# Optimization experiments

Hardware: AMD Instinct MI355X
Metric: run time of the kernel (lower is better)

The kernel has to match this reference:

```python
import jax, jax.numpy as jnp
import numpy as np

B, S, D, H = 1, 4096, 1024, 16
HD = D // H  # head_dim = 64


def setup_inputs() -> dict:
    key = jax.random.key(0)
    k1, k2, k3 = jax.random.split(key, 3)
    scale = 0.02
    return {
        "x": jax.random.normal(k1, (B, S, D), dtype=jnp.float32),
        "w_qkv": jax.random.normal(k2, (D, 3 * D), dtype=jnp.float32) * scale,
        "b_qkv": jnp.zeros((3 * D,), dtype=jnp.float32),
        "w_proj": jax.random.normal(k3, (D, D), dtype=jnp.float32) * scale,
        "b_proj": jnp.zeros((D,), dtype=jnp.float32),
    }


def reference(x, w_qkv, b_qkv, w_proj, b_proj):
    b, s, d = x.shape
    qkv = x @ w_qkv + b_qkv                      # [b, s, 3d]
    q, k, v = jnp.split(qkv, 3, axis=-1)
    # [b, h, s, hd]
    q = q.reshape(b, s, H, HD).transpose(0, 2, 1, 3)
    k = k.reshape(b, s, H, HD).transpose(0, 2, 1, 3)
    v = v.reshape(b, s, H, HD).transpose(0, 2, 1, 3)
    score = jnp.einsum("bhqd,bhkd->bhqk", q, k) / jnp.sqrt(jnp.float32(HD))
    causal = jnp.tril(jnp.ones((s, s), dtype=bool))
    score = jnp.where(causal, score, -jnp.inf)
    attn = jax.nn.softmax(score, axis=-1)        # dropout omitted (eval mode, p effectively 0)
    out = jnp.einsum("bhqk,bhkd->bhqd", attn, v)  # [b, h, s, hd]
    out = out.transpose(0, 2, 1, 3).reshape(b, s, d)
    return out @ w_proj + b_proj
```

## Files before the change

### kernel.cpp

```cpp
#include <hip/hip_runtime.h>
#include <hip/hip_bf16.h>
#include <math.h>

typedef __bf16 bf16;
typedef __bf16 bf16x8 __attribute__((ext_vector_type(8)));
typedef __bf16 bf16x4 __attribute__((ext_vector_type(4)));
typedef float f32x4 __attribute__((ext_vector_type(4)));

#define S_ 4096
#define D_ 1024
#define H_ 16
#define HD_ 64
#define N3_ 3072
#define NSPLIT 2

typedef const __attribute__((address_space(1))) void* gas1_t;
typedef __attribute__((address_space(3))) void* las3_t;
static __device__ __forceinline__ void g2l16(const void* g, void* l) {
  __builtin_amdgcn_global_load_lds((gas1_t)g, (las3_t)l, 16, 0, 0);
}

__global__ __launch_bounds__(256) void prep_kernel(const float* __restrict__ x,
                                                   bf16* __restrict__ xb,
                                                   const float* __restrict__ w_qkv,
                                                   bf16* __restrict__ wqkvT,
                                                   const float* __restrict__ w_proj,
                                                   bf16* __restrict__ wprojT) {
  __shared__ float t[32][33];
  const int b = blockIdx.x;
  if (b < 4096) {
    int i = (b * 256 + threadIdx.x) * 4;
    float4 v = *(const float4*)(x + i);
    bf16x4 o;
    o.x = (bf16)v.x; o.y = (bf16)v.y; o.z = (bf16)v.z; o.w = (bf16)v.w;
    *(bf16x4*)(xb + i) = o;
    return;
  }
  const float* in; bf16* outp; int ldin, bx, by;
  if (b < 7168) { int b2 = b - 4096; in = w_qkv;  outp = wqkvT;  ldin = N3_; bx = (b2 % 96) * 32; by = (b2 / 96) * 32; }
  else          { int b3 = b - 7168; in = w_proj; outp = wprojT; ldin = D_;  bx = (b3 % 32) * 32; by = (b3 / 32) * 32; }
  const int tx = threadIdx.x & 31, ty = threadIdx.x >> 5;
#pragma unroll
  for (int i = 0; i < 4; ++i)
    t[ty + i * 8][tx] = in[(size_t)(by + ty + i * 8) * ldin + bx + tx];
  __syncthreads();
#pragma unroll
  for (int i = 0; i < 4; ++i)
    outp[(size_t)(bx + ty + i * 8) * D_ + by + tx] = (bf16)t[tx][ty + i * 8];
}

__global__ __launch_bounds__(512, 2) void gemm256_qkv(const bf16* __restrict__ A,
                                                      const bf16* __restrict__ Bt,
                                                      const float* __restrict__ bias,
                                                      bf16* __restrict__ outb,
                                                      bf16* __restrict__ vTout,
                                                      float qscale) {
  __shared__ bf16 smem[65536];
  const int K = D_;
  const int NTK = K / 64;
  const int tid = threadIdx.x;
  const int lane = tid & 63, wv = tid >> 6;
  const int col = lane & 15, quad = lane >> 4;
  const int wr = wv >> 2, wc = wv & 3;
  const long bm = (long)blockIdx.x * 256, bn = (long)blockIdx.y * 256;

  int srowA[2][2], srowB[2][2];
  int schA[2][2], schB[2][2];
#pragma unroll
  for (int q = 0; q < 2; ++q) {
    int slot = q * 512 + tid;
    int rl = slot >> 3, ch = slot & 7;
#pragma unroll
    for (int h = 0; h < 2; ++h) {
      int rowA = (rl & 63) | (h << 6) | ((rl >> 6) << 7);
      srowA[h][q] = rowA; schA[h][q] = ch ^ (rowA & 7);
      int rowB = (rl & 31) | (h << 5) | ((rl >> 5) << 6);
      srowB[h][q] = rowB; schB[h][q] = ch ^ (rowB & 7);
    }
  }
  const int dstoff = tid * 8;

  const int ck[2] = { ((0 * 4 + quad) ^ (col & 7)) * 8, ((1 * 4 + quad) ^ (col & 7)) * 8 };

#define STAGE_A(h, T, buf)                                                        \
  {                                                                               \
    const int kbs = (T) * 64;                                                     \
    bf16* lb = smem + (buf) * 32768 + (h) * 8192;                                 \
    g2l16(A + (bm + srowA[h][0]) * (long)K + kbs + schA[h][0] * 8, lb + dstoff);  \
    g2l16(A + (bm + srowA[h][1]) * (long)K + kbs + schA[h][1] * 8, lb + 4096 + dstoff); \
  }
#define STAGE_B(h, T, buf)                                                        \
  {                                                                               \
    const int kbs = (T) * 64;                                                     \
    bf16* lb = smem + (buf) * 32768 + 16384 + (h) * 8192;                         \
    g2l16(Bt + (bn + srowB[h][0]) * (long)K + kbs + schB[h][0] * 8, lb + dstoff); \
    g2l16(Bt + (bn + srowB[h][1]) * (long)K + kbs + schB[h][1] * 8, lb + 4096 + dstoff); \
  }

  f32x4 acc[8][4] = {};

  STAGE_A(0, 0, 0);
  STAGE_A(1, 0, 0);
  STAGE_B(0, 0, 0);
  STAGE_A(0, 1, 1);
  STAGE_B(1, 0, 0);

  for (int G = 0; G < NTK; ++G) {
    const int cur = G & 1;
    const bf16* bufc = smem + cur * 32768;
    const bool last = (G == NTK - 1);

    bf16x8 afr[4][2], bfr[2][2][2];

    if (last) asm volatile("s_waitcnt vmcnt(2)" ::: "memory");
    else      asm volatile("s_waitcnt vmcnt(4)" ::: "memory");
    __builtin_amdgcn_s_barrier();
    __builtin_amdgcn_sched_barrier(0);
#pragma unroll
    for (int mt = 0; mt < 4; ++mt) {
      const bf16* rp = bufc + (wr * 64 + mt * 16 + col) * 64;
      afr[mt][0] = *(const bf16x8*)(rp + ck[0]);
      afr[mt][1] = *(const bf16x8*)(rp + ck[1]);
    }
#pragma unroll
    for (int nt = 0; nt < 2; ++nt) {
      const bf16* rp = bufc + 16384 + (wc * 32 + nt * 16 + col) * 64;
      bfr[0][nt][0] = *(const bf16x8*)(rp + ck[0]);
      bfr[0][nt][1] = *(const bf16x8*)(rp + ck[1]);
    }
    if (G + 1 < NTK) STAGE_A(1, G + 1, cur ^ 1);
    asm volatile("s_waitcnt lgkmcnt(0)" ::: "memory");
    __builtin_amdgcn_sched_barrier(0);
    __builtin_amdgcn_s_setprio(1);
#pragma unroll
    for (int mt = 0; mt < 4; ++mt)
#pragma unroll
      for (int nt = 0; nt < 2; ++nt) {
        acc[mt][nt] = __builtin_amdgcn_mfma_f32_16x16x32_bf16(afr[mt][0], bfr[0][nt][0], acc[mt][nt], 0, 0, 0);
        acc[mt][nt] = __builtin_amdgcn_mfma_f32_16x16x32_bf16(afr[mt][1], bfr[0][nt][1], acc[mt][nt], 0, 0, 0);
      }
    __builtin_amdgcn_s_setprio(0);

    if (last) asm volatile("s_waitcnt vmcnt(0)" ::: "memory");
    else      asm volatile("s_waitcnt vmcnt(2)" ::: "memory");
    __builtin_amdgcn_s_barrier();
    __builtin_amdgcn_sched_barrier(0);
#pragma unroll
    for (int nt = 0; nt < 2; ++nt) {
      const bf16* rp = bufc + 16384 + 8192 + (wc * 32 + nt * 16 + col) * 64;
      bfr[1][nt][0] = *(const bf16x8*)(rp + ck[0]);
      bfr[1][nt][1] = *(const bf16x8*)(rp + ck[1]);
    }
    if (G + 1 < NTK) STAGE_B(0, G + 1, cur ^ 1);
    asm volatile("s_waitcnt lgkmcnt(0)" ::: "memory");
    __builtin_amdgcn_sched_barrier(0);
    __builtin_amdgcn_s_setprio(1);
#pragma unroll
    for (int mt = 0; mt < 4; ++mt)
#pragma unroll
      for (int nt = 0; nt < 2; ++nt) {
        acc[mt][2 + nt] = __builtin_amdgcn_mfma_f32_16x16x32_bf16(afr[mt][0], bfr[1][nt][0], acc[mt][2 + nt], 0, 0, 0);
        acc[mt][2 + nt] = __builtin_amdgcn_mfma_f32_16x16x32_bf16(afr[mt][1], bfr[1][nt][1], acc[mt][2 + nt], 0, 0, 0);
      }
    __builtin_amdgcn_s_setprio(0);

    __builtin_amdgcn_s_barrier();
    __builtin_amdgcn_sched_barrier(0);
#pragma unroll
    for (int mt = 0; mt < 4; ++mt) {
      const bf16* rp = bufc + 8192 + (wr * 64 + mt * 16 + col) * 64;
      afr[mt][0] = *(const bf16x8*)(rp + ck[0]);
      afr[mt][1] = *(const bf16x8*)(rp + ck[1]);
    }
    if (G + 2 < NTK) STAGE_A(0, G + 2, cur);
    asm volatile("s_waitcnt lgkmcnt(0)" ::: "memory");
    __builtin_amdgcn_sched_barrier(0);
    __builtin_amdgcn_s_setprio(1);
#pragma unroll
    for (int mt = 0; mt < 4; ++mt)
#pragma unroll
      for (int nt = 0; nt < 2; ++nt) {
        acc[4 + mt][2 + nt] = __builtin_amdgcn_mfma_f32_16x16x32_bf16(afr[mt][0], bfr[1][nt][0], acc[4 + mt][2 + nt], 0, 0, 0);
        acc[4 + mt][2 + nt] = __builtin_amdgcn_mfma_f32_16x16x32_bf16(afr[mt][1], bfr[1][nt][1], acc[4 + mt][2 + nt], 0, 0, 0);
      }
    __builtin_amdgcn_s_setprio(0);

    __builtin_amdgcn_s_barrier();
    __builtin_amdgcn_sched_barrier(0);
    if (G + 1 < NTK) STAGE_B(1, G + 1, cur ^ 1);
    __builtin_amdgcn_s_setprio(1);
#pragma unroll
    for (int mt = 0; mt < 4; ++mt)
#pragma unroll
      for (int nt = 0; nt < 2; ++nt) {
        acc[4 + mt][nt] = __builtin_amdgcn_mfma_f32_16x16x32_bf16(afr[mt][0], bfr[0][nt][0], acc[4 + mt][nt], 0, 0, 0);
        acc[4 + mt][nt] = __builtin_amdgcn_mfma_f32_16x16x32_bf16(afr[mt][1], bfr[0][nt][1], acc[4 + mt][nt], 0, 0, 0);
      }
    __builtin_amdgcn_s_setprio(0);
  }

  const bool isV = (blockIdx.y >= 8);
  const bool isQ = (blockIdx.y < 4);
#pragma unroll
  for (int mh = 0; mh < 2; ++mh)
#pragma unroll
    for (int mt = 0; mt < 4; ++mt)
#pragma unroll
      for (int nh = 0; nh < 2; ++nh)
#pragma unroll
        for (int nt = 0; nt < 2; ++nt) {
          long gn = bn + wc * 64 + nh * 32 + nt * 16 + col;
          float bv = bias[gn];
          long gm0 = bm + wr * 128 + mh * 64 + mt * 16 + quad * 4;
          f32x4 a = acc[mh * 4 + mt][nh * 2 + nt];
          if (isV) {
            bf16x4 vv;
#pragma unroll
            for (int i = 0; i < 4; ++i) vv[i] = (bf16)(a[i] + bv);
            *(bf16x4*)(&vTout[(gn - 2 * D_) * (long)S_ + gm0]) = vv;
          } else {
            float sc = isQ ? qscale : 1.0f;
#pragma unroll
            for (int i = 0; i < 4; ++i)
              outb[(gm0 + i) * (long)N3_ + gn] = (bf16)((a[i] + bv) * sc);
          }
        }
#undef STAGE_A
#undef STAGE_B
}

__device__ __forceinline__ int swz_g(int row) {
  return (row & 3) | ((((row >> 2) ^ (row >> 3)) & 1) << 2);
}

__global__ __launch_bounds__(256) void attn_kernel(const bf16* __restrict__ qkv,
                                                   const bf16* __restrict__ vT,
                                                   bf16* __restrict__ Opart,
                                                   float* __restrict__ lws) {
  __shared__ bf16 sK[4][64 * 64];
  __shared__ bf16 sV[4][64 * 64];
  const int bid = blockIdx.x;
  const int wgid = (bid & 7) * 128 + (bid >> 3);
  const int hh = wgid >> 6;
  const int rem = wgid & 63;
  const int qb = 31 - (rem >> 1);
  const int sp = rem & 1;
  const int tid = threadIdx.x;
  const int wave = tid >> 6, lane = tid & 63;
  const int col = lane & 15, quad = lane >> 4;
  const int qbase = qb * 128 + wave * 32;

  const bf16* qp0 = qkv + (size_t)(qbase + col) * N3_ + hh * HD_;
  bf16x8 aq[2][2];
  aq[0][0] = *(const bf16x8*)(qp0 + quad * 8);
  aq[0][1] = *(const bf16x8*)(qp0 + 32 + quad * 8);
  aq[1][0] = *(const bf16x8*)(qp0 + 16 * N3_ + quad * 8);
  aq[1][1] = *(const bf16x8*)(qp0 + 16 * N3_ + 32 + quad * 8);

  bf16x8 ones;
#pragma unroll
  for (int j = 0; j < 8; ++j) ones[j] = (bf16)1.0f;

  f32x4 acc[2][4] = {};
  f32x4 acc_l[2] = {};

  const bf16* kgbase = qkv + D_ + hh * HD_;
  const bf16* vgbase = vT + (size_t)hh * HD_ * S_;
  const int krow = (col >> 2) * 8 + (col & 3);
  const int niter = 2 * (qb + 1);
  const int len = niter / NSPLIT;
  const int it0 = sp * len;
  const int it1 = it0 + len;

  const int srow = tid >> 2;
  const int sc0 = (tid & 3) * 2;
  const int gs = swz_g(srow);
  const int soff0 = srow * 64 + ((sc0 ^ gs) * 8);
  const int soff1 = srow * 64 + (((sc0 + 1) ^ gs) * 8);

  {
    const bf16* kg = kgbase + (size_t)(it0 * 64 + srow) * N3_ + sc0 * 8;
    const bf16* vg = vgbase + (size_t)srow * S_ + it0 * 64 + sc0 * 8;
    *(int4*)(&sK[0][soff0]) = *(const int4*)kg;
    *(int4*)(&sK[0][soff1]) = *(const int4*)(kg + 8);
    *(int4*)(&sV[0][soff0]) = *(const int4*)vg;
    *(int4*)(&sV[0][soff1]) = *(const int4*)(vg + 8);
    if (it0 + 1 < it1) {
      const bf16* kg1 = kg + (size_t)64 * N3_;
      const bf16* vg1 = vg + 64;
      *(int4*)(&sK[1][soff0]) = *(const int4*)kg1;
      *(int4*)(&sK[1][soff1]) = *(const int4*)(kg1 + 8);
      *(int4*)(&sV[1][soff0]) = *(const int4*)vg1;
      *(int4*)(&sV[1][soff1]) = *(const int4*)(vg1 + 8);
    }
  }
  __syncthreads();

#define CHUNK_BODY(KB, BI)                                                        \
  if ((KB) < qbase + 32) {                                                        \
    const bool act0 = (KB) < qbase + 16;                                          \
    const bf16* kc = &sK[BI][0];                                                  \
    const bf16* vc = &sV[BI][0];                                                  \
    f32x4 st[2][4];                                                               \
    _Pragma("unroll")                                                             \
    for (int t = 0; t < 4; ++t) {                                                 \
      int row = (t >> 1) * 32 + (t & 1) * 4 + krow;                               \
      int pc = quad ^ swz_g(row);                                                 \
      bf16x8 kf0 = *(const bf16x8*)(kc + row * 64 + pc * 8);                      \
      bf16x8 kf1 = *(const bf16x8*)(kc + row * 64 + (pc ^ 4) * 8);                \
      if (act0) {                                                                 \
        f32x4 z = {};                                                             \
        z = __builtin_amdgcn_mfma_f32_16x16x32_bf16(kf0, aq[0][0], z, 0, 0, 0);   \
        st[0][t] = __builtin_amdgcn_mfma_f32_16x16x32_bf16(kf1, aq[0][1], z, 0, 0, 0); \
      }                                                                           \
      f32x4 z = {};                                                               \
      z = __builtin_amdgcn_mfma_f32_16x16x32_bf16(kf0, aq[1][0], z, 0, 0, 0);     \
      st[1][t] = __builtin_amdgcn_mfma_f32_16x16x32_bf16(kf1, aq[1][1], z, 0, 0, 0); \
    }                                                                             \
    bf16x8 pfrag[2][2];                                                           \
    _Pragma("unroll")                                                             \
    for (int s2 = 0; s2 < 2; ++s2) {                                              \
      if (s2 == 0 && !act0) continue;                                             \
      const int rowbase = qbase + 16 * s2;                                        \
      float p[4][4];                                                              \
      if ((KB) + 63 <= rowbase) {                                                 \
        _Pragma("unroll")                                                         \
        for (int t = 0; t < 4; ++t)                                               \
          _Pragma("unroll")                                                       \
          for (int r = 0; r < 4; ++r)                                             \
            p[t][r] = __builtin_amdgcn_exp2f(st[s2][t][r]);                       \
      } else {                                                                    \
        _Pragma("unroll")                                                         \
        for (int t = 0; t < 4; ++t)                                               \
          _Pragma("unroll")                                                       \
          for (int r = 0; r < 4; ++r) {                                           \
            int key = (KB) + (t >> 1) * 32 + quad * 8 + (t & 1) * 4 + r;          \
            p[t][r] = (key > rowbase + col) ? 0.f                                 \
                                            : __builtin_amdgcn_exp2f(st[s2][t][r]); \
          }                                                                       \
      }                                                                           \
      _Pragma("unroll")                                                           \
      for (int c = 0; c < 2; ++c)                                                 \
        _Pragma("unroll")                                                         \
        for (int j2 = 0; j2 < 4; ++j2) {                                          \
          pfrag[s2][c][j2]     = (bf16)p[2 * c][j2];                              \
          pfrag[s2][c][j2 + 4] = (bf16)p[2 * c + 1][j2];                          \
        }                                                                         \
    }                                                                             \
    _Pragma("unroll")                                                             \
    for (int c = 0; c < 2; ++c) {                                                 \
      _Pragma("unroll")                                                           \
      for (int n = 0; n < 4; ++n) {                                               \
        int row = n * 16 + col;                                                   \
        int pc = (4 * c + quad) ^ swz_g(row);                                     \
        bf16x8 vf = *(const bf16x8*)(vc + row * 64 + pc * 8);                     \
        if (act0)                                                                 \
          acc[0][n] = __builtin_amdgcn_mfma_f32_16x16x32_bf16(pfrag[0][c], vf, acc[0][n], 0, 0, 0); \
        acc[1][n] = __builtin_amdgcn_mfma_f32_16x16x32_bf16(pfrag[1][c], vf, acc[1][n], 0, 0, 0);   \
      }                                                                           \
      if (act0)                                                                   \
        acc_l[0] = __builtin_amdgcn_mfma_f32_16x16x32_bf16(pfrag[0][c], ones, acc_l[0], 0, 0, 0);   \
      acc_l[1] = __builtin_amdgcn_mfma_f32_16x16x32_bf16(pfrag[1][c], ones, acc_l[1], 0, 0, 0);     \
    }                                                                             \
  }

  for (int j0 = it0; j0 < it1; j0 += 2) {
    const int bb = (((j0 - it0) >> 1) & 1) * 2;
    const bool hasB = (j0 + 1 < it1);
    const bool pfA = (j0 + 2 < it1);
    const bool pfB = (j0 + 3 < it1);

    int4 nk00, nk01, nv00, nv01, nk10, nk11, nv10, nv11;
    if (pfA) {
      const bf16* kg = kgbase + (size_t)((j0 + 2) * 64 + srow) * N3_ + sc0 * 8;
      const bf16* vg = vgbase + (size_t)srow * S_ + (j0 + 2) * 64 + sc0 * 8;
      nk00 = *(const int4*)kg; nk01 = *(const int4*)(kg + 8);
      nv00 = *(const int4*)vg; nv01 = *(const int4*)(vg + 8);
    }
    if (pfB) {
      const bf16* kg = kgbase + (size_t)((j0 + 3) * 64 + srow) * N3_ + sc0 * 8;
      const bf16* vg = vgbase + (size_t)srow * S_ + (j0 + 3) * 64 + sc0 * 8;
      nk10 = *(const int4*)kg; nk11 = *(const int4*)(kg + 8);
      nv10 = *(const int4*)vg; nv11 = *(const int4*)(vg + 8);
    }

    {
      const int kb0 = j0 * 64;
      CHUNK_BODY(kb0, bb);
    }
    if (hasB) {
      const int kb1 = (j0 + 1) * 64;
      CHUNK_BODY(kb1, bb + 1);
    }

    if (pfA) {
      bf16* kn = &sK[bb ^ 2][0];
      bf16* vn = &sV[bb ^ 2][0];
      *(int4*)(kn + soff0) = nk00; *(int4*)(kn + soff1) = nk01;
      *(int4*)(vn + soff0) = nv00; *(int4*)(vn + soff1) = nv01;
    }
    if (pfB) {
      bf16* kn = &sK[(bb ^ 2) + 1][0];
      bf16* vn = &sV[(bb ^ 2) + 1][0];
      *(int4*)(kn + soff0) = nk10; *(int4*)(kn + soff1) = nk11;
      *(int4*)(vn + soff0) = nv10; *(int4*)(vn + soff1) = nv11;
    }
    __syncthreads();
  }
#undef CHUNK_BODY

  bf16* Op = Opart + (size_t)sp * S_ * D_;
#pragma unroll
  for (int s2 = 0; s2 < 2; ++s2) {
    const int rowbase = qbase + 16 * s2;
    if (col == 0) {
#pragma unroll
      for (int r = 0; r < 4; ++r)
        lws[((size_t)sp * H_ + hh) * S_ + rowbase + quad * 4 + r] = acc_l[s2][r];
    }
#pragma unroll
    for (int n = 0; n < 4; ++n)
#pragma unroll
      for (int r = 0; r < 4; ++r)
        Op[(size_t)(rowbase + quad * 4 + r) * D_ + hh * HD_ + n * 16 + col] =
            (bf16)acc[s2][n][r];
  }
}

__global__ __launch_bounds__(256) void attn_combine(const bf16* __restrict__ Opart,
                                                    const float* __restrict__ lws,
                                                    bf16* __restrict__ outb) {
  int e = (blockIdx.x * 256 + threadIdx.x) * 8;
  int s = e >> 10;
  int h = (e & (D_ - 1)) >> 6;
  float l = 0.f;
#pragma unroll
  for (int sp = 0; sp < NSPLIT; ++sp) l += lws[((size_t)sp * H_ + h) * S_ + s];
  float inv = 1.0f / l;
  float o[8] = {};
#pragma unroll
  for (int sp = 0; sp < NSPLIT; ++sp) {
    bf16x8 a = *(const bf16x8*)(Opart + (size_t)sp * S_ * D_ + e);
#pragma unroll
    for (int j = 0; j < 8; ++j) o[j] += (float)a[j];
  }
  bf16x8 r;
#pragma unroll
  for (int j = 0; j < 8; ++j) r[j] = (bf16)(o[j] * inv);
  *(bf16x8*)(outb + e) = r;
}

__global__ __launch_bounds__(256, 2) void proj8_gemm(const bf16* __restrict__ A,
                                                     const bf16* __restrict__ Bt,
                                                     const float* __restrict__ bias,
                                                     float* __restrict__ outf) {
  __shared__ bf16 smem[32768];
  const int K = D_;
  const int NTK = K / 64;
  const int tid = threadIdx.x;
  const int lane = tid & 63, wv = tid >> 6;
  const int col = lane & 15, quad = lane >> 4;
  const int wr = wv >> 1, wc = wv & 1;
  const long bm = (long)blockIdx.x * 128, bn = (long)blockIdx.y * 128;

  int srow[2][2], sch[2][2];
#pragma unroll
  for (int q = 0; q < 2; ++q) {
    int slot = q * 256 + tid;
    int rl = slot >> 3, ch = slot & 7;
#pragma unroll
    for (int h = 0; h < 2; ++h) {
      int row = (rl & 31) | (h << 5) | ((rl >> 5) << 6);
      srow[h][q] = row; sch[h][q] = ch ^ (row & 7);
    }
  }
  const int dstoff = tid * 8;

  const int ck[2] = { ((0 * 4 + quad) ^ (col & 7)) * 8, ((1 * 4 + quad) ^ (col & 7)) * 8 };

#define STAGE_PA(h, T, buf)                                                      \
  {                                                                              \
    const int kbs = (T) * 64;                                                    \
    bf16* lb = smem + (buf) * 16384 + (h) * 4096;                                \
    g2l16(A + (bm + srow[h][0]) * (long)K + kbs + sch[h][0] * 8, lb + dstoff);   \
    g2l16(A + (bm + srow[h][1]) * (long)K + kbs + sch[h][1] * 8, lb + 2048 + dstoff); \
  }
#define STAGE_PB(h, T, buf)                                                      \
  {                                                                              \
    const int kbs = (T) * 64;                                                    \
    bf16* lb = smem + (buf) * 16384 + 8192 + (h) * 4096;                         \
    g2l16(Bt + (bn + srow[h][0]) * (long)K + kbs + sch[h][0] * 8, lb + dstoff);  \
    g2l16(Bt + (bn + srow[h][1]) * (long)K + kbs + sch[h][1] * 8, lb + 2048 + dstoff); \
  }

  f32x4 acc[4][4] = {};

  STAGE_PA(0, 0, 0);
  STAGE_PA(1, 0, 0);
  STAGE_PB(0, 0, 0);
  STAGE_PA(0, 1, 1);
  STAGE_PB(1, 0, 0);

  for (int G = 0; G < NTK; ++G) {
    const int cur = G & 1;
    const bf16* bufc = smem + cur * 16384;
    const bool last = (G == NTK - 1);

    bf16x8 afr[2][2], bfr[2][2][2];

    if (last) asm volatile("s_waitcnt vmcnt(2)" ::: "memory");
    else      asm volatile("s_waitcnt vmcnt(4)" ::: "memory");
    __builtin_amdgcn_s_barrier();
    __builtin_amdgcn_sched_barrier(0);
#pragma unroll
    for (int mt = 0; mt < 2; ++mt) {
      const bf16* rp = bufc + (wr * 32 + mt * 16 + col) * 64;
      afr[mt][0] = *(const bf16x8*)(rp + ck[0]);
      afr[mt][1] = *(const bf16x8*)(rp + ck[1]);
    }
#pragma unroll
    for (int nt = 0; nt < 2; ++nt) {
      const bf16* rp = bufc + 8192 + (wc * 32 + nt * 16 + col) * 64;
      bfr[0][nt][0] = *(const bf16x8*)(rp + ck[0]);
      bfr[0][nt][1] = *(const bf16x8*)(rp + ck[1]);
    }
    if (G + 1 < NTK) STAGE_PA(1, G + 1, cur ^ 1);
    asm volatile("s_waitcnt lgkmcnt(0)" ::: "memory");
    __builtin_amdgcn_sched_barrier(0);
    __builtin_amdgcn_s_setprio(1);
#pragma unroll
    for (int mt = 0; mt < 2; ++mt)
#pragma unroll
      for (int nt = 0; nt < 2; ++nt) {
        acc[mt][nt] = __builtin_amdgcn_mfma_f32_16x16x32_bf16(afr[mt][0], bfr[0][nt][0], acc[mt][nt], 0, 0, 0);
        acc[mt][nt] = __builtin_amdgcn_mfma_f32_16x16x32_bf16(afr[mt][1], bfr[0][nt][1], acc[mt][nt], 0, 0, 0);
      }
    __builtin_amdgcn_s_setprio(0);

    if (last) asm volatile("s_waitcnt vmcnt(0)" ::: "memory");
    else      asm volatile("s_waitcnt vmcnt(2)" ::: "memory");
    __builtin_amdgcn_s_barrier();
    __builtin_amdgcn_sched_barrier(0);
#pragma unroll
    for (int nt = 0; nt < 2; ++nt) {
      const bf16* rp = bufc + 8192 + 4096 + (wc * 32 + nt * 16 + col) * 64;
      bfr[1][nt][0] = *(const bf16x8*)(rp + ck[0]);
      bfr[1][nt][1] = *(const bf16x8*)(rp + ck[1]);
    }
    if (G + 1 < NTK) STAGE_PB(0, G + 1, cur ^ 1);
    asm volatile("s_waitcnt lgkmcnt(0)" ::: "memory");
    __builtin_amdgcn_sched_barrier(0);
    __builtin_amdgcn_s_setprio(1);
#pragma unroll
    for (int mt = 0; mt < 2; ++mt)
#pragma unroll
      for (int nt = 0; nt < 2; ++nt) {
        acc[mt][2 + nt] = __builtin_amdgcn_mfma_f32_16x16x32_bf16(afr[mt][0], bfr[1][nt][0], acc[mt][2 + nt], 0, 0, 0);
        acc[mt][2 + nt] = __builtin_amdgcn_mfma_f32_16x16x32_bf16(afr[mt][1], bfr[1][nt][1], acc[mt][2 + nt], 0, 0, 0);
      }
    __builtin_amdgcn_s_setprio(0);

    __builtin_amdgcn_s_barrier();
    __builtin_amdgcn_sched_barrier(0);
#pragma unroll
    for (int mt = 0; mt < 2; ++mt) {
      const bf16* rp = bufc + 4096 + (wr * 32 + mt * 16 + col) * 64;
      afr[mt][0] = *(const bf16x8*)(rp + ck[0]);
      afr[mt][1] = *(const bf16x8*)(rp + ck[1]);
    }
    if (G + 2 < NTK) STAGE_PA(0, G + 2, cur);
    asm volatile("s_waitcnt lgkmcnt(0)" ::: "memory");
    __builtin_amdgcn_sched_barrier(0);
    __builtin_amdgcn_s_setprio(1);
#pragma unroll
    for (int mt = 0; mt < 2; ++mt)
#pragma unroll
      for (int nt = 0; nt < 2; ++nt) {
        acc[2 + mt][2 + nt] = __builtin_amdgcn_mfma_f32_16x16x32_bf16(afr[mt][0], bfr[1][nt][0], acc[2 + mt][2 + nt], 0, 0, 0);
        acc[2 + mt][2 + nt] = __builtin_amdgcn_mfma_f32_16x16x32_bf16(afr[mt][1], bfr[1][nt][1], acc[2 + mt][2 + nt], 0, 0, 0);
      }
    __builtin_amdgcn_s_setprio(0);

    __builtin_amdgcn_s_barrier();
    __builtin_amdgcn_sched_barrier(0);
    if (G + 1 < NTK) STAGE_PB(1, G + 1, cur ^ 1);
    __builtin_amdgcn_s_setprio(1);
#pragma unroll
    for (int mt = 0; mt < 2; ++mt)
#pragma unroll
      for (int nt = 0; nt < 2; ++nt) {
        acc[2 + mt][nt] = __builtin_amdgcn_mfma_f32_16x16x32_bf16(afr[mt][0], bfr[0][nt][0], acc[2 + mt][nt], 0, 0, 0);
        acc[2 + mt][nt] = __builtin_amdgcn_mfma_f32_16x16x32_bf16(afr[mt][1], bfr[0][nt][1], acc[2 + mt][nt], 0, 0, 0);
      }
    __builtin_amdgcn_s_setprio(0);
  }

#pragma unroll
  for (int mh = 0; mh < 2; ++mh)
#pragma unroll
    for (int mt = 0; mt < 2; ++mt)
#pragma unroll
      for (int nh = 0; nh < 2; ++nh)
#pragma unroll
        for (int nt = 0; nt < 2; ++nt) {
          long gn = bn + wc * 64 + nh * 32 + nt * 16 + col;
          float bv = bias[gn];
          long gm0 = bm + wr * 64 + mh * 32 + mt * 16 + quad * 4;
          f32x4 a = acc[mh * 2 + mt][nh * 2 + nt];
#pragma unroll
          for (int i = 0; i < 4; ++i)
            outf[(gm0 + i) * (long)D_ + gn] = a[i] + bv;
        }
#undef STAGE_PA
#undef STAGE_PB
}

extern "C" void kernel_launch(void* const* d_in, const int* in_sizes, int n_in,
                              void* d_out, int out_size, void* d_ws, size_t ws_size,
                              hipStream_t stream) {
  const float* x      = (const float*)d_in[0];
  const float* w_qkv  = (const float*)d_in[1];
  const float* b_qkv  = (const float*)d_in[2];
  const float* w_proj = (const float*)d_in[3];
  const float* b_proj = (const float*)d_in[4];
  float* out = (float*)d_out;

  bf16* xb     = (bf16*)d_ws;
  bf16* wqkvT  = xb + (size_t)S_ * D_;
  bf16* wprojT = wqkvT + (size_t)N3_ * D_;
  bf16* qkv    = wprojT + (size_t)D_ * D_;
  bf16* vT     = qkv + (size_t)S_ * N3_;
  bf16* Opart  = vT + (size_t)D_ * S_;
  float* lws   = (float*)(Opart + (size_t)NSPLIT * S_ * D_);
  bf16* attn   = xb;

  const float QSCALE = 0.125f * 1.44269504088896f;

  prep_kernel<<<dim3(8192), 256, 0, stream>>>(x, xb, w_qkv, wqkvT, w_proj, wprojT);
  gemm256_qkv<<<dim3(S_ / 256, N3_ / 256), 512, 0, stream>>>(
      xb, wqkvT, b_qkv, qkv, vT, QSCALE);
  attn_kernel<<<dim3(1024), 256, 0, stream>>>(qkv, vT, Opart, lws);
  attn_combine<<<dim3((S_ * D_) / 2048), 256, 0, stream>>>(Opart, lws, attn);
  proj8_gemm<<<dim3(S_ / 128, D_ / 128), 256, 0, stream>>>(
      attn, wprojT, b_proj, out);
}
```

Before: 189.7 us.

## Fuse split-KV combine into attention kernel via atomic ticket counter

Removes the separate attn_combine launch. Each attention workgroup takes an atomic ticket per (head, query-block) after writing its partial output, and the second finisher normalises and sums both splits into the final attention buffer. Counters are zeroed in the prep kernel. This saves a kernel launch and its full pass over memory, at the cost of threadfences, an atomic, and a serialized tail in the last-arriving workgroup.

New measurement: 371.6 us. 1.96x slower.

```diff
diff --git a/kernel.cpp b/kernel.cpp
--- a/kernel.cpp
+++ b/kernel.cpp
@@ -25,7 +25,8 @@
                                                    const float* __restrict__ w_qkv,
                                                    bf16* __restrict__ wqkvT,
                                                    const float* __restrict__ w_proj,
-                                                   bf16* __restrict__ wprojT) {
+                                                   bf16* __restrict__ wprojT,
+                                                   int* __restrict__ cnt) {
   __shared__ float t[32][33];
   const int b = blockIdx.x;
   if (b < 4096) {
@@ -35,6 +36,10 @@
     o.x = (bf16)v.x; o.y = (bf16)v.y; o.z = (bf16)v.z; o.w = (bf16)v.w;
     *(bf16x4*)(xb + i) = o;
     return;
+  }
+  if (b == 8191) {
+    cnt[threadIdx.x] = 0;
+    cnt[threadIdx.x + 256] = 0;
   }
   const float* in; bf16* outp; int ldin, bx, by;
   if (b < 7168) { int b2 = b - 4096; in = w_qkv;  outp = wqkvT;  ldin = N3_; bx = (b2 % 96) * 32; by = (b2 / 96) * 32; }
@@ -236,9 +241,12 @@
 __global__ __launch_bounds__(256) void attn_kernel(const bf16* __restrict__ qkv,
                                                    const bf16* __restrict__ vT,
                                                    bf16* __restrict__ Opart,
-                                                   float* __restrict__ lws) {
+                                                   float* __restrict__ lws,
+                                                   bf16* __restrict__ outb,
+                                                   int* __restrict__ cnt) {
   __shared__ bf16 sK[4][64 * 64];
   __shared__ bf16 sV[4][64 * 64];
+  __shared__ int ticket;
   const int bid = blockIdx.x;
   const int wgid = (bid & 7) * 128 + (bid >> 3);
   const int hh = wgid >> 6;
@@ -425,29 +433,30 @@
         Op[(size_t)(rowbase + quad * 4 + r) * D_ + hh * HD_ + n * 16 + col] =
             (bf16)acc[s2][n][r];
   }
-}
-
-__global__ __launch_bounds__(256) void attn_combine(const bf16* __restrict__ Opart,
-                                                    const float* __restrict__ lws,
-                                                    bf16* __restrict__ outb) {
-  int e = (blockIdx.x * 256 + threadIdx.x) * 8;
-  int s = e >> 10;
-  int h = (e & (D_ - 1)) >> 6;
-  float l = 0.f;
-#pragma unroll
-  for (int sp = 0; sp < NSPLIT; ++sp) l += lws[((size_t)sp * H_ + h) * S_ + s];
-  float inv = 1.0f / l;
-  float o[8] = {};
-#pragma unroll
-  for (int sp = 0; sp < NSPLIT; ++sp) {
-    bf16x8 a = *(const bf16x8*)(Opart + (size_t)sp * S_ * D_ + e);
-#pragma unroll
-    for (int j = 0; j < 8; ++j) o[j] += (float)a[j];
-  }
-  bf16x8 r;
-#pragma unroll
-  for (int j = 0; j < 8; ++j) r[j] = (bf16)(o[j] * inv);
-  *(bf16x8*)(outb + e) = r;
+
+  __threadfence();
+  if (tid == 0) ticket = atomicAdd(&cnt[hh * 32 + qb], 1);
+  __syncthreads();
+  if (ticket == 1) {
+    __threadfence();
+    const int r = tid >> 1;
+    const int cb = (tid & 1) * 32;
+    const int row = qb * 128 + r;
+    const float l = lws[(size_t)hh * S_ + row] +
+                    lws[((size_t)H_ + hh) * S_ + row];
+    const float inv = 1.0f / l;
+    const size_t base = (size_t)row * D_ + hh * HD_ + cb;
+#pragma unroll
+    for (int cc = 0; cc < 4; ++cc) {
+      bf16x8 a0 = *(const bf16x8*)(Opart + base + cc * 8);
+      bf16x8 a1 = *(const bf16x8*)(Opart + (size_t)S_ * D_ + base + cc * 8);
+      bf16x8 r8;
+#pragma unroll
+      for (int j = 0; j < 8; ++j)
+        r8[j] = (bf16)(((float)a0[j] + (float)a1[j]) * inv);
+      *(bf16x8*)(outb + base + cc * 8) = r8;
+    }
+  }
 }
 
 __global__ __launch_bounds__(256, 2) void proj8_gemm(const bf16* __restrict__ A,
@@ -632,15 +641,15 @@
   bf16* vT     = qkv + (size_t)S_ * N3_;
   bf16* Opart  = vT + (size_t)D_ * S_;
   float* lws   = (float*)(Opart + (size_t)NSPLIT * S_ * D_);
+  int*   cnt   = (int*)(lws + (size_t)NSPLIT * H_ * S_);
   bf16* attn   = xb;
 
   const float QSCALE = 0.125f * 1.44269504088896f;
 
-  prep_kernel<<<dim3(8192), 256, 0, stream>>>(x, xb, w_qkv, wqkvT, w_proj, wprojT);
+  prep_kernel<<<dim3(8192), 256, 0, stream>>>(x, xb, w_qkv, wqkvT, w_proj, wprojT, cnt);
   gemm256_qkv<<<dim3(S_ / 256, N3_ / 256), 512, 0, stream>>>(
       xb, wqkvT, b_qkv, qkv, vT, QSCALE);
-  attn_kernel<<<dim3(1024), 256, 0, stream>>>(qkv, vT, Opart, lws);
-  attn_combine<<<dim3((S_ * D_) / 2048), 256, 0, stream>>>(Opart, lws, attn);
+  attn_kernel<<<dim3(1024), 256, 0, stream>>>(qkv, vT, Opart, lws, attn, cnt);
   proj8_gemm<<<dim3(S_ / 128, D_ / 128), 256, 0, stream>>>(
       attn, wprojT, b_proj, out);
 }
```
